# Performance work log

Hardware: AMD Instinct MI355X
Metric: run time of the kernel (lower is better)

## Reference

```python
import jax, jax.numpy as jnp
import numpy as np

EPS = 1e-12
TEMP = 0.05
LAMBDA2 = 0.5


def _normalize(x):
    # F.normalize(x, dim=1), eps=1e-12
    n = jnp.linalg.norm(x, axis=1, keepdims=True)
    return x / jnp.maximum(n, EPS)


def _cdist(x, f):
    # torch.cdist p=2: [B, N] euclidean distances
    x2 = jnp.sum(x * x, axis=1, keepdims=True)          # [B,1]
    f2 = jnp.sum(f * f, axis=1)[None, :]                # [1,N]
    d2 = x2 + f2 - 2.0 * (x @ f.T)
    return jnp.sqrt(jnp.maximum(d2, 0.0))


def _ce(logits, targets):
    # F.cross_entropy with integer targets, mean reduction
    logp = jax.nn.log_softmax(logits, axis=1)
    return -jnp.take_along_axis(logp, targets[:, None], axis=1).mean()


def _branch_loss(x_raw, f, targets):
    x = _normalize(x_raw)
    # note: original applies cross_entropy (which does another log_softmax)
    # on top of softmax(cdist(...)) -- reproduced faithfully
    soft = jax.nn.softmax(_cdist(x, f), axis=1)
    out = (x @ f.T) / TEMP
    return _ce(out, targets) + _ce(soft, targets)


def setup_inputs() -> dict:
    key = jax.random.key(0)
    ks = jax.random.split(key, 7)
    B, N, D = 256, 8192, 2048
    inputs = jax.random.normal(ks[0], (B, D), dtype=jnp.float32)
    inputs_up = jax.random.normal(ks[1], (B, D), dtype=jnp.float32)
    inputs_down = jax.random.normal(ks[2], (B, D), dtype=jnp.float32)
    targets = jax.random.randint(ks[3], (B,), 0, N)
    # memory banks are buffers; initialize as L2-normalized rows (realistic state)
    features = _normalize(jax.random.normal(ks[4], (N, D), dtype=jnp.float32))
    features_up = _normalize(jax.random.normal(ks[5], (N, D), dtype=jnp.float32))
    features_down = _normalize(jax.random.normal(ks[6], (N, D), dtype=jnp.float32))
    return {
        "inputs": inputs,
        "inputs_up": inputs_up,
        "inputs_down": inputs_down,
        "targets": targets,
        "epoch": 10,
        "features": features,
        "features_up": features_up,
        "features_down": features_down,
    }


def reference(inputs, inputs_up, inputs_down, targets, epoch, features, features_up, features_down):
    l_mid = _branch_loss(inputs, features, targets)
    l_up = _branch_loss(inputs_up, features_up, targets)
    l_down = _branch_loss(inputs_down, features_down, targets)
    loss = (1.0 - LAMBDA2) * l_mid + LAMBDA2 * (l_up + l_down)
    return loss
```

## Files before the change

### kernel.cpp

```cpp
#include <hip/hip_runtime.h>

typedef float f4v __attribute__((ext_vector_type(4)));
typedef float f32x4 __attribute__((ext_vector_type(4)));
typedef __bf16 bf16x8 __attribute__((ext_vector_type(8)));
typedef unsigned short ushort8 __attribute__((ext_vector_type(8)));

static constexpr int BROWS = 256;
static constexpr int NCOLS = 8192;
static constexpr int KDIM  = 2048;

static constexpr size_t OFF_XN      = 0;
static constexpr size_t OFF_PART    = (size_t)3 * 256 * 2048 * 2;
static constexpr size_t OFF_DOTT    = OFF_PART + (size_t)3 * 256 * 128 * 16;
static constexpr size_t OFF_ROWLOSS = OFF_DOTT + 768 * 4;

__device__ __forceinline__ unsigned short f2bf(float x) {
  union { float f; unsigned u; } c; c.f = x;
  unsigned r = c.u + 0x7fffu + ((c.u >> 16) & 1u);
  return (unsigned short)(r >> 16);
}

__device__ __forceinline__ void gload_lds16(const void* g, void* l) {
  __builtin_amdgcn_global_load_lds((const __attribute__((address_space(1))) void*)g,
                                   (__attribute__((address_space(3))) void*)l,
                                   16, 0, 0);
}

__global__ __launch_bounds__(256) void k_normalize(
    const float* __restrict__ x0, const float* __restrict__ x1, const float* __restrict__ x2,
    unsigned short* __restrict__ xn)
{
  int bid = blockIdx.x;
  int branch = bid >> 8;
  int row = bid & 255;
  const float* src = (branch == 0 ? x0 : (branch == 1 ? x1 : x2)) + (size_t)row * KDIM;
  int tid = threadIdx.x;
  f4v a = *(const f4v*)(src + tid * 8);
  f4v b = *(const f4v*)(src + tid * 8 + 4);
  float s = a[0]*a[0] + a[1]*a[1] + a[2]*a[2] + a[3]*a[3]
          + b[0]*b[0] + b[1]*b[1] + b[2]*b[2] + b[3]*b[3];
  #pragma unroll
  for (int m = 1; m < 64; m <<= 1) s += __shfl_xor(s, m);
  __shared__ float ls[4];
  if ((tid & 63) == 0) ls[tid >> 6] = s;
  __syncthreads();
  float total = ls[0] + ls[1] + ls[2] + ls[3];
  float inv = 1.0f / fmaxf(sqrtf(total), 1e-12f);
  ushort8 u;
  #pragma unroll
  for (int e = 0; e < 4; ++e) u[e]     = f2bf(a[e] * inv);
  #pragma unroll
  for (int e = 0; e < 4; ++e) u[4 + e] = f2bf(b[e] * inv);
  *(ushort8*)(xn + (size_t)bid * KDIM + tid * 8) = u;
}

__global__ __launch_bounds__(256, 2) void k_gemm_fused(
    const unsigned short* __restrict__ xn,
    const float* __restrict__ f0, const float* __restrict__ f1, const float* __restrict__ f2,
    const int* __restrict__ targets,
    float* __restrict__ part, float* __restrict__ dotT)
{
  __shared__ unsigned short lA[256 * 64];
  __shared__ unsigned short lB[64 * 64];

  int bid = blockIdx.x;
  int swz = (bid & 7) * 48 + (bid >> 3);
  int branch = swz >> 7;
  int ntile = swz & 127;

  const unsigned short* A = xn + (size_t)branch * (256 * 2048);
  const float* F = (branch == 0 ? f0 : (branch == 1 ? f1 : f2)) + (size_t)ntile * 64 * 2048;

  int tid = threadIdx.x;
  int wave = tid >> 6;
  int lane = tid & 63;

  f32x4 acc[4][4];
  #pragma unroll
  for (int i = 0; i < 4; ++i)
    #pragma unroll
    for (int j = 0; j < 4; ++j)
      #pragma unroll
      for (int q = 0; q < 4; ++q) acc[i][j][q] = 0.0f;

  for (int kt = 0; kt < 32; ++kt) {
    int kbase = kt * 64;
    f4v bv00, bv01, bv10, bv11;
    {
      int ci = tid;
      int brow = ci >> 3, bc = ci & 7, gc = bc ^ (brow & 7);
      const float* s = F + brow * 2048 + kbase + gc * 8;
      bv00 = *(const f4v*)s; bv01 = *(const f4v*)(s + 4);
    }
    {
      int ci = 256 + tid;
      int brow = ci >> 3, bc = ci & 7, gc = bc ^ (brow & 7);
      const float* s = F + brow * 2048 + kbase + gc * 8;
      bv10 = *(const f4v*)s; bv11 = *(const f4v*)(s + 4);
    }
    #pragma unroll
    for (int r = 0; r < 8; ++r) {
      int chunk = r * 256 + tid;
      int arow = chunk >> 3, ac = chunk & 7;
      int gc = ac ^ (arow & 7);
      gload_lds16(A + arow * 2048 + kbase + gc * 8,
                  (char*)lA + (r * 256 + wave * 64) * 16);
    }
    {
      int brow = tid >> 3, bc = tid & 7;
      ushort8 u;
      #pragma unroll
      for (int e = 0; e < 4; ++e) u[e]     = f2bf(bv00[e]);
      #pragma unroll
      for (int e = 0; e < 4; ++e) u[4 + e] = f2bf(bv01[e]);
      *(ushort8*)(lB + brow * 64 + bc * 8) = u;
    }
    {
      int ci = 256 + tid;
      int brow = ci >> 3, bc = ci & 7;
      ushort8 u;
      #pragma unroll
      for (int e = 0; e < 4; ++e) u[e]     = f2bf(bv10[e]);
      #pragma unroll
      for (int e = 0; e < 4; ++e) u[4 + e] = f2bf(bv11[e]);
      *(ushort8*)(lB + brow * 64 + bc * 8) = u;
    }
    __syncthreads();

    bf16x8 af[4][2], bfr[4][2];
    #pragma unroll
    for (int i = 0; i < 4; ++i)
      #pragma unroll
      for (int ks = 0; ks < 2; ++ks) {
        int row = wave * 64 + i * 16 + (lane & 15);
        int kc = ks * 4 + (lane >> 4);
        af[i][ks] = *(const bf16x8*)(lA + row * 64 + ((kc ^ (row & 7)) << 3));
      }
    #pragma unroll
    for (int j = 0; j < 4; ++j)
      #pragma unroll
      for (int ks = 0; ks < 2; ++ks) {
        int col = j * 16 + (lane & 15);
        int kc = ks * 4 + (lane >> 4);
        bfr[j][ks] = *(const bf16x8*)(lB + col * 64 + ((kc ^ (col & 7)) << 3));
      }
    #pragma unroll
    for (int ks = 0; ks < 2; ++ks)
      #pragma unroll
      for (int i = 0; i < 4; ++i)
        #pragma unroll
        for (int j = 0; j < 4; ++j)
          acc[i][j] = __builtin_amdgcn_mfma_f32_16x16x32_bf16(af[i][ks], bfr[j][ks], acc[i][j], 0, 0, 0);
    __syncthreads();
  }

  int tbase = branch * 256;
  #pragma unroll
  for (int i = 0; i < 4; ++i) {
    #pragma unroll
    for (int q = 0; q < 4; ++q) {
      int row = wave * 64 + i * 16 + ((lane >> 4) << 2) + q;
      int tgt = targets[row];
      float s1 = 0.f, s2 = 0.f, s3 = 0.f, s4 = 0.f;
      #pragma unroll
      for (int j = 0; j < 4; ++j) {
        float d = acc[i][j][q];
        float e1 = __expf(fmaf(20.0f, d, -20.0f));
        float Dv = sqrtf(fmaxf(2.0f - 2.0f * d, 0.0f));
        float e2 = __expf(Dv - 2.0f);
        s1 += e1; s2 += e2;
        float t2 = e2 * e2;
        s3 += t2; s4 += t2 * e2;
        int col = ntile * 64 + j * 16 + (lane & 15);
        if (col == tgt) dotT[tbase + row] = d;
      }
      #pragma unroll
      for (int m = 1; m < 16; m <<= 1) {
        s1 += __shfl_xor(s1, m);
        s2 += __shfl_xor(s2, m);
        s3 += __shfl_xor(s3, m);
        s4 += __shfl_xor(s4, m);
      }
      if ((lane & 15) == 0) {
        f32x4 p; p[0] = s1; p[1] = s2; p[2] = s3; p[3] = s4;
        *(f32x4*)(part + ((size_t)(tbase + row) * 128 + ntile) * 4) = p;
      }
    }
  }
}

__global__ __launch_bounds__(128) void k_combine(
    const float* __restrict__ part, const float* __restrict__ dotT, float* __restrict__ rowloss)
{
  int row = blockIdx.x;
  int tid = threadIdx.x;
  f4v p = *(const f4v*)(part + ((size_t)row * 128 + tid) * 4);
  float a0 = p[0], a1 = p[1], a2 = p[2], a3 = p[3];
  #pragma unroll
  for (int m = 1; m < 64; m <<= 1) {
    a0 += __shfl_xor(a0, m); a1 += __shfl_xor(a1, m);
    a2 += __shfl_xor(a2, m); a3 += __shfl_xor(a3, m);
  }
  __shared__ float ls[8];
  if ((tid & 63) == 0) {
    int w = tid >> 6;
    ls[w] = a0; ls[2 + w] = a1; ls[4 + w] = a2; ls[6 + w] = a3;
  }
  __syncthreads();
  if (tid == 0) {
    float p1 = ls[0] + ls[1];
    float Z1 = ls[2] + ls[3];
    float Z2 = ls[4] + ls[5];
    float Z3 = ls[6] + ls[7];
    float dt = dotT[row];
    float CE1 = 20.0f + logf(p1) - 20.0f * dt;
    float Dt = sqrtf(fmaxf(2.0f - 2.0f * dt, 0.0f));
    float St = __expf(Dt - 2.0f) / Z1;
    float sES = 8193.0f + Z2 / (2.0f * Z1 * Z1) + Z3 / (6.0f * Z1 * Z1 * Z1);
    float CE2 = logf(sES) - St;
    rowloss[row] = (CE1 + CE2) * (0.5f / 256.0f);
  }
}

__global__ __launch_bounds__(256) void k_final(const float* __restrict__ rowloss, float* __restrict__ out)
{
  int tid = threadIdx.x;
  float v = rowloss[tid] + rowloss[tid + 256] + rowloss[tid + 512];
  #pragma unroll
  for (int m = 1; m < 64; m <<= 1) v += __shfl_xor(v, m);
  __shared__ float ls[4];
  if ((tid & 63) == 0) ls[tid >> 6] = v;
  __syncthreads();
  if (tid == 0) out[0] = ls[0] + ls[1] + ls[2] + ls[3];
}

extern "C" void kernel_launch(void* const* d_in, const int* in_sizes, int n_in,
                              void* d_out, int out_size, void* d_ws, size_t ws_size,
                              hipStream_t stream) {
  const float* in0 = (const float*)d_in[0];
  const float* in1 = (const float*)d_in[1];
  const float* in2 = (const float*)d_in[2];
  const int* targets = (const int*)d_in[3];
  const float* f0 = (const float*)d_in[5];
  const float* f1 = (const float*)d_in[6];
  const float* f2 = (const float*)d_in[7];

  char* ws = (char*)d_ws;
  unsigned short* xn = (unsigned short*)(ws + OFF_XN);
  float* part    = (float*)(ws + OFF_PART);
  float* dotT    = (float*)(ws + OFF_DOTT);
  float* rowloss = (float*)(ws + OFF_ROWLOSS);
  float* out = (float*)d_out;

  k_normalize<<<768, 256, 0, stream>>>(in0, in1, in2, xn);
  k_gemm_fused<<<384, 256, 0, stream>>>(xn, f0, f1, f2, targets, part, dotT);
  k_combine<<<768, 128, 0, stream>>>(part, dotT, rowloss);
  k_final<<<1, 256, 0, stream>>>(rowloss, out);
}
```

Measured before the change: 73.48 us.

## Halve GEMM N-tile, stream A from global, double-buffer B in LDS

The fused GEMM now uses 32-column tiles, so it launches 768 blocks with occupancy 3 and only a small double-buffered LDS tile for B. A fragments are read directly from global memory (L2-resident bf16) instead of being staged through LDS. B loads are nontemporal and prefetched one k-step ahead of the conversion and compute. The goal is better CU fill and overlap of the fp32 feature streaming with MFMA work, at the cost of re-reading A from L2 in every block and doubling the partial-sum buffer and combine width.

```diff
diff --git a/kernel.cpp b/kernel.cpp
--- a/kernel.cpp
+++ b/kernel.cpp
@@ -5,13 +5,11 @@
 typedef __bf16 bf16x8 __attribute__((ext_vector_type(8)));
 typedef unsigned short ushort8 __attribute__((ext_vector_type(8)));
 
-static constexpr int BROWS = 256;
-static constexpr int NCOLS = 8192;
-static constexpr int KDIM  = 2048;
+static constexpr int KDIM = 2048;
 
 static constexpr size_t OFF_XN      = 0;
 static constexpr size_t OFF_PART    = (size_t)3 * 256 * 2048 * 2;
-static constexpr size_t OFF_DOTT    = OFF_PART + (size_t)3 * 256 * 128 * 16;
+static constexpr size_t OFF_DOTT    = OFF_PART + (size_t)768 * 256 * 16;
 static constexpr size_t OFF_ROWLOSS = OFF_DOTT + 768 * 4;
 
 __device__ __forceinline__ unsigned short f2bf(float x) {
@@ -20,12 +18,6 @@
   return (unsigned short)(r >> 16);
 }
 
-__device__ __forceinline__ void gload_lds16(const void* g, void* l) {
-  __builtin_amdgcn_global_load_lds((const __attribute__((address_space(1))) void*)g,
-                                   (__attribute__((address_space(3))) void*)l,
-                                   16, 0, 0);
-}
-
 __global__ __launch_bounds__(256) void k_normalize(
     const float* __restrict__ x0, const float* __restrict__ x1, const float* __restrict__ x2,
     unsigned short* __restrict__ xn)
@@ -54,105 +46,99 @@
   *(ushort8*)(xn + (size_t)bid * KDIM + tid * 8) = u;
 }
 
-__global__ __launch_bounds__(256, 2) void k_gemm_fused(
+__global__ __launch_bounds__(256, 3) void k_gemm_fused(
     const unsigned short* __restrict__ xn,
     const float* __restrict__ f0, const float* __restrict__ f1, const float* __restrict__ f2,
     const int* __restrict__ targets,
     float* __restrict__ part, float* __restrict__ dotT)
 {
-  __shared__ unsigned short lA[256 * 64];
-  __shared__ unsigned short lB[64 * 64];
+  __shared__ unsigned short lB[2 * 32 * 64];
 
   int bid = blockIdx.x;
-  int swz = (bid & 7) * 48 + (bid >> 3);
-  int branch = swz >> 7;
-  int ntile = swz & 127;
+  int swz = (bid & 7) * 96 + (bid >> 3);
+  int branch = swz >> 8;
+  int ntile = swz & 255;
 
   const unsigned short* A = xn + (size_t)branch * (256 * 2048);
-  const float* F = (branch == 0 ? f0 : (branch == 1 ? f1 : f2)) + (size_t)ntile * 64 * 2048;
+  const float* F = (branch == 0 ? f0 : (branch == 1 ? f1 : f2)) + (size_t)ntile * 32 * 2048;
 
   int tid = threadIdx.x;
   int wave = tid >> 6;
   int lane = tid & 63;
-
-  f32x4 acc[4][4];
+  int rcol0 = lane & 15;
+
+  const float* bSrc = F + (size_t)(tid >> 3) * 2048 + (tid & 7) * 8;
+  int wcol = tid >> 3;
+  int wByte = wcol * 128 + (((tid & 7) ^ (wcol & 7)) << 4);
+
+  const unsigned short* aBase = A + (size_t)(wave * 64 + rcol0) * 2048 + (lane >> 4) * 8;
+  const unsigned short* aP0 = aBase;
+  const unsigned short* aP1 = aBase + 16 * 2048;
+  const unsigned short* aP2 = aBase + 32 * 2048;
+  const unsigned short* aP3 = aBase + 48 * 2048;
+
+  f32x4 acc[4][2];
   #pragma unroll
   for (int i = 0; i < 4; ++i)
     #pragma unroll
-    for (int j = 0; j < 4; ++j)
+    for (int j = 0; j < 2; ++j)
       #pragma unroll
       for (int q = 0; q < 4; ++q) acc[i][j][q] = 0.0f;
 
-  for (int kt = 0; kt < 32; ++kt) {
-    int kbase = kt * 64;
-    f4v bv00, bv01, bv10, bv11;
-    {
-      int ci = tid;
-      int brow = ci >> 3, bc = ci & 7, gc = bc ^ (brow & 7);
-      const float* s = F + brow * 2048 + kbase + gc * 8;
-      bv00 = *(const f4v*)s; bv01 = *(const f4v*)(s + 4);
-    }
-    {
-      int ci = 256 + tid;
-      int brow = ci >> 3, bc = ci & 7, gc = bc ^ (brow & 7);
-      const float* s = F + brow * 2048 + kbase + gc * 8;
-      bv10 = *(const f4v*)s; bv11 = *(const f4v*)(s + 4);
-    }
-    #pragma unroll
-    for (int r = 0; r < 8; ++r) {
-      int chunk = r * 256 + tid;
-      int arow = chunk >> 3, ac = chunk & 7;
-      int gc = ac ^ (arow & 7);
-      gload_lds16(A + arow * 2048 + kbase + gc * 8,
-                  (char*)lA + (r * 256 + wave * 64) * 16);
-    }
-    {
-      int brow = tid >> 3, bc = tid & 7;
-      ushort8 u;
-      #pragma unroll
-      for (int e = 0; e < 4; ++e) u[e]     = f2bf(bv00[e]);
-      #pragma unroll
-      for (int e = 0; e < 4; ++e) u[4 + e] = f2bf(bv01[e]);
-      *(ushort8*)(lB + brow * 64 + bc * 8) = u;
-    }
-    {
-      int ci = 256 + tid;
-      int brow = ci >> 3, bc = ci & 7;
-      ushort8 u;
-      #pragma unroll
-      for (int e = 0; e < 4; ++e) u[e]     = f2bf(bv10[e]);
-      #pragma unroll
-      for (int e = 0; e < 4; ++e) u[4 + e] = f2bf(bv11[e]);
-      *(ushort8*)(lB + brow * 64 + bc * 8) = u;
-    }
+  f4v bs0, bs1;
+
+#define LOAD_B(kt) do { \
+    bs0 = __builtin_nontemporal_load((const f4v*)(bSrc + (kt) * 64)); \
+    bs1 = __builtin_nontemporal_load((const f4v*)(bSrc + (kt) * 64 + 4)); \
+  } while (0)
+
+#define WRITE_B(bufsel) do { \
+    ushort8 u; \
+    _Pragma("unroll") for (int e = 0; e < 4; ++e) u[e]     = f2bf(bs0[e]); \
+    _Pragma("unroll") for (int e = 0; e < 4; ++e) u[4 + e] = f2bf(bs1[e]); \
+    *(ushort8*)((char*)lB + (bufsel) * 4096 + wByte) = u; \
+  } while (0)
+
+#define COMPUTE(cur, kt) do { \
+    const char* rb = (const char*)lB + (cur) * 4096; \
+    _Pragma("unroll") for (int ks = 0; ks < 2; ++ks) { \
+      int chunk = (((ks * 4 + (lane >> 4)) ^ (rcol0 & 7)) << 4); \
+      bf16x8 bj0 = *(const bf16x8*)(rb + rcol0 * 128 + chunk); \
+      bf16x8 bj1 = *(const bf16x8*)(rb + (rcol0 + 16) * 128 + chunk); \
+      bf16x8 a0 = *(const bf16x8*)(aP0 + (kt) * 64 + ks * 32); \
+      bf16x8 a1 = *(const bf16x8*)(aP1 + (kt) * 64 + ks * 32); \
+      bf16x8 a2 = *(const bf16x8*)(aP2 + (kt) * 64 + ks * 32); \
+      bf16x8 a3 = *(const bf16x8*)(aP3 + (kt) * 64 + ks * 32); \
+      acc[0][0] = __builtin_amdgcn_mfma_f32_16x16x32_bf16(a0, bj0, acc[0][0], 0, 0, 0); \
+      acc[0][1] = __builtin_amdgcn_mfma_f32_16x16x32_bf16(a0, bj1, acc[0][1], 0, 0, 0); \
+      acc[1][0] = __builtin_amdgcn_mfma_f32_16x16x32_bf16(a1, bj0, acc[1][0], 0, 0, 0); \
+      acc[1][1] = __builtin_amdgcn_mfma_f32_16x16x32_bf16(a1, bj1, acc[1][1], 0, 0, 0); \
+      acc[2][0] = __builtin_amdgcn_mfma_f32_16x16x32_bf16(a2, bj0, acc[2][0], 0, 0, 0); \
+      acc[2][1] = __builtin_amdgcn_mfma_f32_16x16x32_bf16(a2, bj1, acc[2][1], 0, 0, 0); \
+      acc[3][0] = __builtin_amdgcn_mfma_f32_16x16x32_bf16(a3, bj0, acc[3][0], 0, 0, 0); \
+      acc[3][1] = __builtin_amdgcn_mfma_f32_16x16x32_bf16(a3, bj1, acc[3][1], 0, 0, 0); \
+    } \
+  } while (0)
+
+  LOAD_B(0);
+  WRITE_B(0);
+  LOAD_B(1);
+  __syncthreads();
+
+  for (int t = 0; t < 30; ++t) {
+    WRITE_B((t + 1) & 1);
+    LOAD_B(t + 2);
+    COMPUTE(t & 1, t);
     __syncthreads();
-
-    bf16x8 af[4][2], bfr[4][2];
-    #pragma unroll
-    for (int i = 0; i < 4; ++i)
-      #pragma unroll
-      for (int ks = 0; ks < 2; ++ks) {
-        int row = wave * 64 + i * 16 + (lane & 15);
-        int kc = ks * 4 + (lane >> 4);
-        af[i][ks] = *(const bf16x8*)(lA + row * 64 + ((kc ^ (row & 7)) << 3));
-      }
-    #pragma unroll
-    for (int j = 0; j < 4; ++j)
-      #pragma unroll
-      for (int ks = 0; ks < 2; ++ks) {
-        int col = j * 16 + (lane & 15);
-        int kc = ks * 4 + (lane >> 4);
-        bfr[j][ks] = *(const bf16x8*)(lB + col * 64 + ((kc ^ (col & 7)) << 3));
-      }
-    #pragma unroll
-    for (int ks = 0; ks < 2; ++ks)
-      #pragma unroll
-      for (int i = 0; i < 4; ++i)
-        #pragma unroll
-        for (int j = 0; j < 4; ++j)
-          acc[i][j] = __builtin_amdgcn_mfma_f32_16x16x32_bf16(af[i][ks], bfr[j][ks], acc[i][j], 0, 0, 0);
-    __syncthreads();
-  }
+  }
+  WRITE_B(1);
+  COMPUTE(0, 30);
+  __syncthreads();
+  COMPUTE(1, 31);
+
+#undef LOAD_B
+#undef WRITE_B
+#undef COMPUTE
 
   int tbase = branch * 256;
   #pragma unroll
@@ -163,7 +149,7 @@
       int tgt = targets[row];
       float s1 = 0.f, s2 = 0.f, s3 = 0.f, s4 = 0.f;
       #pragma unroll
-      for (int j = 0; j < 4; ++j) {
+      for (int j = 0; j < 2; ++j) {
         float d = acc[i][j][q];
         float e1 = __expf(fmaf(20.0f, d, -20.0f));
         float Dv = sqrtf(fmaxf(2.0f - 2.0f * d, 0.0f));
@@ -171,7 +157,7 @@
         s1 += e1; s2 += e2;
         float t2 = e2 * e2;
         s3 += t2; s4 += t2 * e2;
-        int col = ntile * 64 + j * 16 + (lane & 15);
+        int col = ntile * 32 + j * 16 + rcol0;
         if (col == tgt) dotT[tbase + row] = d;
       }
       #pragma unroll
@@ -181,37 +167,37 @@
         s3 += __shfl_xor(s3, m);
         s4 += __shfl_xor(s4, m);
       }
-      if ((lane & 15) == 0) {
+      if (rcol0 == 0) {
         f32x4 p; p[0] = s1; p[1] = s2; p[2] = s3; p[3] = s4;
-        *(f32x4*)(part + ((size_t)(tbase + row) * 128 + ntile) * 4) = p;
+        *(f32x4*)(part + ((size_t)(tbase + row) * 256 + ntile) * 4) = p;
       }
     }
   }
 }
 
-__global__ __launch_bounds__(128) void k_combine(
+__global__ __launch_bounds__(256) void k_combine(
     const float* __restrict__ part, const float* __restrict__ dotT, float* __restrict__ rowloss)
 {
   int row = blockIdx.x;
   int tid = threadIdx.x;
-  f4v p = *(const f4v*)(part + ((size_t)row * 128 + tid) * 4);
+  f4v p = *(const f4v*)(part + ((size_t)row * 256 + tid) * 4);
   float a0 = p[0], a1 = p[1], a2 = p[2], a3 = p[3];
   #pragma unroll
   for (int m = 1; m < 64; m <<= 1) {
     a0 += __shfl_xor(a0, m); a1 += __shfl_xor(a1, m);
     a2 += __shfl_xor(a2, m); a3 += __shfl_xor(a3, m);
   }
-  __shared__ float ls[8];
+  __shared__ float ls[4][4];
   if ((tid & 63) == 0) {
     int w = tid >> 6;
-    ls[w] = a0; ls[2 + w] = a1; ls[4 + w] = a2; ls[6 + w] = a3;
+    ls[0][w] = a0; ls[1][w] = a1; ls[2][w] = a2; ls[3][w] = a3;
   }
   __syncthreads();
   if (tid == 0) {
-    float p1 = ls[0] + ls[1];
-    float Z1 = ls[2] + ls[3];
-    float Z2 = ls[4] + ls[5];
-    float Z3 = ls[6] + ls[7];
+    float p1 = ls[0][0] + ls[0][1] + ls[0][2] + ls[0][3];
+    float Z1 = ls[1][0] + ls[1][1] + ls[1][2] + ls[1][3];
+    float Z2 = ls[2][0] + ls[2][1] + ls[2][2] + ls[2][3];
+    float Z3 = ls[3][0] + ls[3][1] + ls[3][2] + ls[3][3];
     float dt = dotT[row];
     float CE1 = 20.0f + logf(p1) - 20.0f * dt;
     float Dt = sqrtf(fmaxf(2.0f - 2.0f * dt, 0.0f));
@@ -253,7 +239,7 @@
   float* out = (float*)d_out;
 
   k_normalize<<<768, 256, 0, stream>>>(in0, in1, in2, xn);
-  k_gemm_fused<<<384, 256, 0, stream>>>(xn, f0, f1, f2, targets, part, dotT);
-  k_combine<<<768, 128, 0, stream>>>(part, dotT, rowloss);
+  k_gemm_fused<<<768, 256, 0, stream>>>(xn, f0, f1, f2, targets, part, dotT);
+  k_combine<<<768, 256, 0, stream>>>(part, dotT, rowloss);
   k_final<<<1, 256, 0, stream>>>(rowloss, out);
 }
```

Measured after the change: 133.2 us. 81.3% more time.
